# Performance work log

Measured on AMD Instinct MI355X. Metric: run time of the kernel, lower is better.

The kernel has to match this reference:

```python
import jax, jax.numpy as jnp
import numpy as np
from jax import lax

H = W = 4096

def _directional_filters():
    f0   = [[0,0,0],[0,1,-1],[0,0,0]]
    f45  = [[0,0,0],[0,1,0],[0,0,-1]]
    f90  = [[0,0,0],[0,1,0],[0,-1,0]]
    f135 = [[0,0,0],[0,1,0],[-1,0,0]]
    f180 = [[0,0,0],[-1,1,0],[0,0,0]]
    f225 = [[-1,0,0],[0,1,0],[0,0,0]]
    f270 = [[0,-1,0],[0,1,0],[0,0,0]]
    f315 = [[0,0,-1],[0,1,0],[0,0,0]]
    w = np.stack([f0,f45,f90,f135,f180,f225,f270,f315]).astype(np.float32)
    return jnp.asarray(w[:, None, :, :])  # [8,1,3,3]

def setup_inputs() -> dict:
    key = jax.random.key(0)
    k1, k2 = jax.random.split(key)
    grad_magnitude = jax.random.uniform(k1, (1, 1, H, W), dtype=jnp.float32)
    # orientation in degrees, quantized to multiples of 45 as in Canny
    grad_orientation = jax.random.randint(k2, (1, 1, H, W), 0, 8).astype(jnp.float32) * 45.0
    weight = _directional_filters()
    bias = jnp.zeros((8,), dtype=jnp.float32)
    return {"grad_magnitude": grad_magnitude, "grad_orientation": grad_orientation,
            "weight": weight, "bias": bias}

def reference(grad_magnitude, grad_orientation, weight, bias):
    # directional 3x3 conv, 1 -> 8 channels, 'SAME' padding
    all_filtered = lax.conv_general_dilated(
        grad_magnitude, weight, window_strides=(1, 1), padding='SAME')
    all_filtered = all_filtered + bias[None, :, None, None]  # [1,8,H,W]
    # per-pixel orientation channel indices (floor matches torch .long())
    idx_pos = jnp.floor(grad_orientation / 45.0).astype(jnp.int32) % 8  # [1,1,H,W]
    idx_neg = (idx_pos + 4) % 8
    f = all_filtered[0]                                  # [8,H,W]
    pos = jnp.take_along_axis(f, idx_pos[0], axis=0)     # [1,H,W]
    neg = jnp.take_along_axis(f, idx_neg[0], axis=0)     # [1,H,W]
    is_max = jnp.minimum(pos, neg) > 0.0                 # [1,H,W]
    thin_edges = jnp.where(is_max[None], grad_magnitude, 0.0)  # [1,1,H,W]
    return thin_edges
```

## Files before the change

kernel.cpp:

```cpp
#include <hip/hip_runtime.h>


constexpr int H = 4096;
constexpr int W = 4096;
constexpr long NPX = (long)H * W;

typedef float v4f __attribute__((ext_vector_type(4)));

__device__ __forceinline__ v4f ldv(const float* __restrict__ p, long idx) {
    return *reinterpret_cast<const v4f*>(p + idx);
}

__global__ __launch_bounds__(256) void nms_kernel(
    const float* __restrict__ mag,
    const float* __restrict__ orient,
    const float* __restrict__ bias,
    float* __restrict__ out)
{
    const int tid = blockIdx.x * 256 + threadIdx.x;
    const int y   = tid >> 10;
    const int x0  = (tid & 1023) << 2;
    const long base = ((long)y << 12) + x0;

    const long ubase = (y > 0)     ? base - W : base;
    const long dbase = (y < H - 1) ? base + W : base;

    const v4f cA = ldv(mag, base);
    const v4f cL = ldv(mag, (base - 4 > 0) ? base - 4 : 0);
    const v4f cR = ldv(mag, (base + 4 < NPX - 4) ? base + 4 : NPX - 4);
    const v4f uA = ldv(mag, ubase);
    const v4f uL = ldv(mag, (ubase - 4 > 0) ? ubase - 4 : 0);
    const v4f uR = ldv(mag, (ubase + 4 < NPX - 4) ? ubase + 4 : NPX - 4);
    const v4f dA = ldv(mag, dbase);
    const v4f dL = ldv(mag, (dbase - 4 > 0) ? dbase - 4 : 0);
    const v4f dR = ldv(mag, (dbase + 4 < NPX - 4) ? dbase + 4 : NPX - 4);
    const v4f o4 = ldv(orient, base);

    float b[8];
    #pragma unroll
    for (int i = 0; i < 8; ++i) b[i] = bias[i];

    const float um = (y > 0)      ? 1.f : 0.f;
    const float dm = (y < H - 1)  ? 1.f : 0.f;
    const float lm = (x0 > 0)     ? 1.f : 0.f;
    const float rm = (x0 + 4 < W) ? 1.f : 0.f;

    const float u6[6] = {uL.w * (um * lm), uA.x * um, uA.y * um,
                         uA.z * um, uA.w * um, uR.x * (um * rm)};
    const float c6[6] = {cL.w * lm, cA.x, cA.y, cA.z, cA.w, cR.x * rm};
    const float d6[6] = {dL.w * (dm * lm), dA.x * dm, dA.y * dm,
                         dA.z * dm, dA.w * dm, dR.x * (dm * rm)};

    const float m[4] = {cA.x, cA.y, cA.z, cA.w};
    const float o[4] = {o4.x, o4.y, o4.z, o4.w};

    float r[4];
    #pragma unroll
    for (int k = 0; k < 4; ++k) {
        const int c = (int)(o[k] * 0.0222222222f + 0.5f);
        const bool b0 = (c & 1), b1 = (c & 2);

        const float M0 = fmaxf(c6[k + 2] - b[0], c6[k]     - b[4]);
        const float M1 = fmaxf(d6[k + 2] - b[1], u6[k]     - b[5]);
        const float M2 = fmaxf(d6[k + 1] - b[2], u6[k + 1] - b[6]);
        const float M3 = fmaxf(d6[k]     - b[3], u6[k + 2] - b[7]);

        const float m01 = b0 ? M1 : M0;
        const float m23 = b0 ? M3 : M2;
        const float Mj  = b1 ? m23 : m01;

        r[k] = (m[k] > Mj) ? m[k] : 0.0f;
    }

    v4f res; res.x = r[0]; res.y = r[1]; res.z = r[2]; res.w = r[3];
    __builtin_nontemporal_store(res, reinterpret_cast<v4f*>(out + base));
}

extern "C" void kernel_launch(void* const* d_in, const int* in_sizes, int n_in,
                              void* d_out, int out_size, void* d_ws, size_t ws_size,
                              hipStream_t stream) {
    const float* mag    = (const float*)d_in[0];
    const float* orient = (const float*)d_in[1];
    const float* bias   = (const float*)d_in[3];
    float* out = (float*)d_out;

    const int total = H * (W / 4);
    dim3 block(256);
    dim3 grid(total / 256);
    hipLaunchKernelGGL(nms_kernel, grid, block, 0, stream,
                       mag, orient, bias, out);
}
```

Measured before the change: 178.5 us.

## Process four rows per thread and map row strips to XCDs for L2 reuse

Each thread now computes a 4x4 output tile, loading 6 magnitude rows once and reusing them across the 4 output rows. Halo columns are fetched as scalar loads instead of full float4 vectors. Block indices are remapped so that contiguous row strips stay on the same XCD, which should improve L2 locality for the vertical halos. The cost is higher register use per thread and one quarter as many threads, which may reduce occupancy and latency hiding in a memory-bound kernel.

```diff
diff --git a/kernel.cpp b/kernel.cpp
--- a/kernel.cpp
+++ b/kernel.cpp
@@ -3,57 +3,15 @@
 
 constexpr int H = 4096;
 constexpr int W = 4096;
-constexpr long NPX = (long)H * W;
 
 typedef float v4f __attribute__((ext_vector_type(4)));
 
-__device__ __forceinline__ v4f ldv(const float* __restrict__ p, long idx) {
-    return *reinterpret_cast<const v4f*>(p + idx);
-}
-
-__global__ __launch_bounds__(256) void nms_kernel(
-    const float* __restrict__ mag,
-    const float* __restrict__ orient,
-    const float* __restrict__ bias,
-    float* __restrict__ out)
+__device__ __forceinline__ v4f nms_quad(const float u6[6], const float c6[6],
+                                        const float d6[6], v4f m4, v4f o4,
+                                        const float b[8])
 {
-    const int tid = blockIdx.x * 256 + threadIdx.x;
-    const int y   = tid >> 10;
-    const int x0  = (tid & 1023) << 2;
-    const long base = ((long)y << 12) + x0;
-
-    const long ubase = (y > 0)     ? base - W : base;
-    const long dbase = (y < H - 1) ? base + W : base;
-
-    const v4f cA = ldv(mag, base);
-    const v4f cL = ldv(mag, (base - 4 > 0) ? base - 4 : 0);
-    const v4f cR = ldv(mag, (base + 4 < NPX - 4) ? base + 4 : NPX - 4);
-    const v4f uA = ldv(mag, ubase);
-    const v4f uL = ldv(mag, (ubase - 4 > 0) ? ubase - 4 : 0);
-    const v4f uR = ldv(mag, (ubase + 4 < NPX - 4) ? ubase + 4 : NPX - 4);
-    const v4f dA = ldv(mag, dbase);
-    const v4f dL = ldv(mag, (dbase - 4 > 0) ? dbase - 4 : 0);
-    const v4f dR = ldv(mag, (dbase + 4 < NPX - 4) ? dbase + 4 : NPX - 4);
-    const v4f o4 = ldv(orient, base);
-
-    float b[8];
-    #pragma unroll
-    for (int i = 0; i < 8; ++i) b[i] = bias[i];
-
-    const float um = (y > 0)      ? 1.f : 0.f;
-    const float dm = (y < H - 1)  ? 1.f : 0.f;
-    const float lm = (x0 > 0)     ? 1.f : 0.f;
-    const float rm = (x0 + 4 < W) ? 1.f : 0.f;
-
-    const float u6[6] = {uL.w * (um * lm), uA.x * um, uA.y * um,
-                         uA.z * um, uA.w * um, uR.x * (um * rm)};
-    const float c6[6] = {cL.w * lm, cA.x, cA.y, cA.z, cA.w, cR.x * rm};
-    const float d6[6] = {dL.w * (dm * lm), dA.x * dm, dA.y * dm,
-                         dA.z * dm, dA.w * dm, dR.x * (dm * rm)};
-
-    const float m[4] = {cA.x, cA.y, cA.z, cA.w};
+    const float m[4] = {m4.x, m4.y, m4.z, m4.w};
     const float o[4] = {o4.x, o4.y, o4.z, o4.w};
-
     float r[4];
     #pragma unroll
     for (int k = 0; k < 4; ++k) {
@@ -71,9 +29,77 @@
 
         r[k] = (m[k] > Mj) ? m[k] : 0.0f;
     }
+    v4f res; res.x = r[0]; res.y = r[1]; res.z = r[2]; res.w = r[3];
+    return res;
+}
 
-    v4f res; res.x = r[0]; res.y = r[1]; res.z = r[2]; res.w = r[3];
-    __builtin_nontemporal_store(res, reinterpret_cast<v4f*>(out + base));
+__global__ __launch_bounds__(256) void nms_kernel(
+    const float* __restrict__ mag,
+    const float* __restrict__ orient,
+    const float* __restrict__ bias,
+    float* __restrict__ out)
+{
+    const int bid   = blockIdx.x;
+    const int xcd   = bid & 7;
+    const int j     = bid >> 3;
+    const int sband = j >> 2;
+    const int bq    = j & 3;
+    const int strip = xcd * 128 + sband;
+
+    const int x0 = (bq * 256 + threadIdx.x) << 2;
+    const int y0 = strip << 2;
+
+    const int   xL = (x0 > 0) ? x0 - 1 : 0;
+    const int   xR = (x0 + 4 < W) ? x0 + 4 : W - 1;
+    const float lm = (x0 > 0) ? 1.f : 0.f;
+    const float rm = (x0 + 4 < W) ? 1.f : 0.f;
+    const float um = (y0 > 0) ? 1.f : 0.f;
+    const float dm = (y0 + 4 < H) ? 1.f : 0.f;
+
+    int rowoff[6];
+    #pragma unroll
+    for (int i = 0; i < 6; ++i) {
+        int r = y0 + i - 1;
+        r = (r < 0) ? 0 : ((r > H - 1) ? H - 1 : r);
+        rowoff[i] = r << 12;
+    }
+
+    v4f  A[6];
+    float Lh[6], Rh[6];
+    #pragma unroll
+    for (int i = 0; i < 6; ++i) {
+        A[i]  = *reinterpret_cast<const v4f*>(mag + rowoff[i] + x0);
+        Lh[i] = mag[rowoff[i] + xL];
+        Rh[i] = mag[rowoff[i] + xR];
+    }
+    v4f O[4];
+    #pragma unroll
+    for (int i = 0; i < 4; ++i)
+        O[i] = *reinterpret_cast<const v4f*>(orient + rowoff[i + 1] + x0);
+
+    float b[8];
+    #pragma unroll
+    for (int i = 0; i < 8; ++i) b[i] = bias[i];
+
+    float Rm[6][6];
+    #pragma unroll
+    for (int i = 0; i < 6; ++i) {
+        const float vm = (i == 0) ? um : ((i == 5) ? dm : 1.f);
+        Rm[i][0] = Lh[i] * (lm * vm);
+        Rm[i][1] = A[i].x * vm;
+        Rm[i][2] = A[i].y * vm;
+        Rm[i][3] = A[i].z * vm;
+        Rm[i][4] = A[i].w * vm;
+        Rm[i][5] = Rh[i] * (rm * vm);
+    }
+
+    #pragma unroll
+    for (int jr = 0; jr < 4; ++jr) {
+        const v4f res = nms_quad(Rm[jr], Rm[jr + 1], Rm[jr + 2],
+                                 A[jr + 1], O[jr], b);
+        __builtin_nontemporal_store(
+            res, reinterpret_cast<v4f*>(out + rowoff[jr + 1] + x0));
+    }
 }
 
 extern "C" void kernel_launch(void* const* d_in, const int* in_sizes, int n_in,
@@ -84,7 +110,7 @@
     const float* bias   = (const float*)d_in[3];
     float* out = (float*)d_out;
 
-    const int total = H * (W / 4);
+    const int total = (H / 4) * (W / 4);
     dim3 block(256);
     dim3 grid(total / 256);
     hipLaunchKernelGGL(nms_kernel, grid, block, 0, stream,
```

Result: no change. 177.8 us (-0.4%).
